# Kernel tuning notes

Measured on AMD Instinct MI355X. Metric: run time of the kernel, lower is better.

Reference implementation:

```python
import jax, jax.numpy as jnp
import numpy as np

WS = 8      # window_size
SS = 4      # shift_size
DIM = 64
B, H, W = 4, 256, 256
EPS = 1e-12


def _conv(x, w, groups=1, pad=0):
    return jax.lax.conv_general_dilated(
        x, w, window_strides=(1, 1), padding=[(pad, pad), (pad, pad)],
        feature_group_count=groups,
        dimension_numbers=('NCHW', 'OIHW', 'NCHW'))


def _window_partition(x, ws):
    # Faithful to torch: permute (B,C,nh,ws,nw,ws)->(B,C,nh,nw,ws,ws) then flat view(-1,C,ws,ws)
    b, c, h, w = x.shape
    pb, pr = (-h) % ws, (-w) % ws
    if pb or pr:
        x = jnp.pad(x, ((0, 0), (0, 0), (0, pb), (0, pr)))
    h2, w2 = h + pb, w + pr
    x = x.reshape(b, c, h2 // ws, ws, w2 // ws, ws).transpose(0, 1, 2, 4, 3, 5)
    return x.reshape(-1, c, ws, ws)


def _window_reverse(win, ws, h, w):
    pb, pr = (-h) % ws, (-w) % ws
    h2, w2 = h + pb, w + pr
    b = win.shape[0] * ws * ws // (h2 * w2)
    x = win.reshape(b, -1, h2 // ws, w2 // ws, ws, ws).transpose(0, 1, 2, 4, 3, 5)
    x = x.reshape(b, -1, h2, w2)
    return x[:, :, :h, :w]


def _chan_attn(q, k, v, temp):
    # channel (transposed) attention on flattened window pixels
    n, c = q.shape[0], q.shape[1]
    q = q.reshape(n, c, -1)
    k = k.reshape(n, c, -1)
    v = v.reshape(n, c, -1)
    q = q / jnp.maximum(jnp.linalg.norm(q, axis=-1, keepdims=True), EPS)
    k = k / jnp.maximum(jnp.linalg.norm(k, axis=-1, keepdims=True), EPS)
    attn = jax.nn.softmax(jnp.einsum('ncd,nkd->nck', q, k) / temp, axis=-1)
    out = jnp.einsum('nck,nkd->ncd', attn, v)
    return out.reshape(n, c, WS, WS)


def setup_inputs() -> dict:
    key = jax.random.key(0)
    ks = jax.random.split(key, 10)
    C = DIM
    p = lambda k, s: jax.random.normal(k, s, jnp.float32) * 0.05
    return {
        'x': jax.random.normal(ks[0], (B, C, H, W), jnp.float32),
        'x_f': jax.random.normal(ks[1], (B, C, H, W), jnp.float32),
        'temperature': jnp.ones((1,), jnp.float32),
        'qk_w': p(ks[2], (2 * C, C, 1, 1)),
        'qk_dw_w': p(ks[3], (2 * C, 1, 3, 3)),
        'v_w': p(ks[4], (C, C, 1, 1)),
        'v_dw_w': p(ks[5], (C, 1, 3, 3)),
        'proj_w': p(ks[6], (C, C, 3, 3)),
        'proj1_w': p(ks[7], (C, C, 3, 3)),
        'qkv1_w': p(ks[8], (3 * C, C, 1, 1)),
        'qkv1_dw_w': p(ks[9], (3 * C, 1, 3, 3)),
    }


def reference(x, x_f, temperature, qk_w, qk_dw_w, v_w, v_dw_w,
              proj_w, proj1_w, qkv1_w, qkv1_dw_w):
    b, c, h, w = x.shape
    xw = _window_partition(x, WS)
    xfw = _window_partition(x_f, WS)

    qk = _conv(_conv(xfw, qk_w), qk_dw_w, groups=2 * c, pad=1)
    v = _conv(_conv(xw, v_w), v_dw_w, groups=c, pad=1)
    q, k = jnp.split(qk, 2, axis=1)
    out = _chan_attn(q, k, v, temperature)
    out = _conv(out, proj_w, pad=1)
    out = _window_reverse(out, WS, h, w)

    shift = jnp.roll(out, (-SS, -SS), axis=(2, 3))
    sw = _window_partition(shift, WS)
    qkv = _conv(_conv(sw, qkv1_w), qkv1_dw_w, groups=3 * c, pad=1)
    q, k, v = jnp.split(qkv, 3, axis=1)
    out = _chan_attn(q, k, v, temperature)
    out = _conv(out, proj1_w, pad=1)
    out = _window_reverse(out, WS, h, w)
    out = jnp.roll(out, (SS, SS), axis=(2, 3))
    return out
```

## Files before the change

### kernel.cpp

```cpp
#include <hip/hip_runtime.h>

typedef short v8s __attribute__((ext_vector_type(8)));
typedef float v4f __attribute__((ext_vector_type(4)));
typedef unsigned short u16;

#define MFMA_B16(a, b, c) __builtin_amdgcn_mfma_f32_16x16x32_bf16((a), (b), (c), 0, 0, 0)
#define XS 72

__device__ __forceinline__ u16 bfr(float x) {
    unsigned u = __float_as_uint(x);
    u += 0x7fffu + ((u >> 16) & 1u);
    return (u16)(u >> 16);
}
__device__ __forceinline__ u16 f16r(float x) {
    _Float16 h = (_Float16)x; u16 u; __builtin_memcpy(&u, &h, 2); return u;
}
__device__ __forceinline__ float f16f(u16 u) {
    _Float16 h; __builtin_memcpy(&h, &u, 2); return (float)h;
}

__device__ __forceinline__ void mm_stage(const u16* __restrict__ Ag,
                                         const u16* __restrict__ XB,
                                         u16* __restrict__ M,
                                         int wv, int L, int q)
{
    v4f C[4];
#pragma unroll
    for (int nt = 0; nt < 4; ++nt) C[nt] = (v4f){0.f, 0.f, 0.f, 0.f};
#pragma unroll
    for (int kt = 0; kt < 2; ++kt) {
        v8s a = *(const v8s*)(Ag + (16 * wv + L) * 64 + kt * 32 + q * 8);
#pragma unroll
        for (int nt = 0; nt < 4; ++nt) {
            v8s b = *(const v8s*)(XB + (nt * 16 + L) * XS + kt * 32 + q * 8);
            C[nt] = MFMA_B16(a, b, C[nt]);
        }
    }
    const int rowb = 16 * wv + 4 * q;
#pragma unroll
    for (int r = 0; r < 4; ++r)
#pragma unroll
        for (int nt = 0; nt < 4; ++nt)
            M[(rowb + r) * XS + nt * 16 + L] = f16r(C[nt][r]);
}

__device__ __forceinline__ void dw_read(const u16* __restrict__ M, int c, int r0,
                                        v8s raw[4])
{
#pragma unroll
    for (int r = 0; r < 4; ++r) {
        const int rr = r0 - 1 + r;
        raw[r] = ((unsigned)rr < 8u) ? *(const v8s*)(M + c * XS + rr * 8)
                                     : (v8s){0, 0, 0, 0, 0, 0, 0, 0};
    }
}

template <bool TR, bool NORM>
__device__ __forceinline__ void dw_write(const float* __restrict__ dwg,
                                         const v8s raw[4], int c, int r0,
                                         u16* __restrict__ Out)
{
    float w[9];
#pragma unroll
    for (int k = 0; k < 9; ++k) w[k] = dwg[c * 9 + k];
    float in[4][10];
#pragma unroll
    for (int r = 0; r < 4; ++r) {
        in[r][0] = 0.f; in[r][9] = 0.f;
#pragma unroll
        for (int j = 0; j < 8; ++j) in[r][j + 1] = f16f((u16)raw[r][j]);
    }
    float o[2][8];
#pragma unroll
    for (int rr = 0; rr < 2; ++rr)
#pragma unroll
        for (int j = 0; j < 8; ++j) {
            float s;
            s = w[0] * in[rr][j];
            s = fmaf(w[1], in[rr][j + 1], s);
            s = fmaf(w[2], in[rr][j + 2], s);
            s = fmaf(w[3], in[rr + 1][j], s);
            s = fmaf(w[4], in[rr + 1][j + 1], s);
            s = fmaf(w[5], in[rr + 1][j + 2], s);
            s = fmaf(w[6], in[rr + 2][j], s);
            s = fmaf(w[7], in[rr + 2][j + 1], s);
            s = fmaf(w[8], in[rr + 2][j + 2], s);
            o[rr][j] = s;
        }
    if (NORM) {
        float ss = 0.f;
#pragma unroll
        for (int rr = 0; rr < 2; ++rr)
#pragma unroll
            for (int j = 0; j < 8; ++j) ss = fmaf(o[rr][j], o[rr][j], ss);
        ss += __shfl_xor(ss, 1);
        ss += __shfl_xor(ss, 2);
        const float sc = 1.0f / fmaxf(sqrtf(ss), 1e-12f);
#pragma unroll
        for (int rr = 0; rr < 2; ++rr)
#pragma unroll
            for (int j = 0; j < 8; ++j) o[rr][j] *= sc;
    }
    if (TR) {
#pragma unroll
        for (int rr = 0; rr < 2; ++rr)
#pragma unroll
            for (int j = 0; j < 8; ++j)
                Out[((r0 + rr) * 8 + j) * XS + c] = bfr(o[rr][j]);
    } else {
#pragma unroll
        for (int rr = 0; rr < 2; ++rr) {
            v8s v;
#pragma unroll
            for (int j = 0; j < 8; ++j) v[j] = (short)bfr(o[rr][j]);
            *(v8s*)(Out + c * XS + (r0 + rr) * 8) = v;
        }
    }
}

__device__ __forceinline__ void mm_lds(const u16* __restrict__ Am,
                                       const u16* __restrict__ Bm,
                                       int wv, int L, int q, v4f C[4])
{
#pragma unroll
    for (int nt = 0; nt < 4; ++nt) C[nt] = (v4f){0.f, 0.f, 0.f, 0.f};
#pragma unroll
    for (int kt = 0; kt < 2; ++kt) {
        v8s a = *(const v8s*)(Am + (16 * wv + L) * XS + kt * 32 + q * 8);
#pragma unroll
        for (int nt = 0; nt < 4; ++nt) {
            v8s b = *(const v8s*)(Bm + (nt * 16 + L) * XS + kt * 32 + q * 8);
            C[nt] = MFMA_B16(a, b, C[nt]);
        }
    }
}

__device__ __forceinline__ void proj_mm(const u16* __restrict__ Wg,
                                        const u16* __restrict__ Ot,
                                        int wv, int L, int q, v4f C[4])
{
#pragma unroll
    for (int nt = 0; nt < 4; ++nt) C[nt] = (v4f){0.f, 0.f, 0.f, 0.f};
    const u16* arow = Wg + (16 * wv + L) * 576;
    const int pc = L & 7;
    const int prb = L >> 3;
#pragma unroll
    for (int tap = 0; tap < 9; ++tap) {
        const int dy = tap / 3 - 1, dx = tap % 3 - 1;
        const int spc = pc + dx;
        const bool vc = (unsigned)spc < 8u;
#pragma unroll
        for (int half = 0; half < 2; ++half) {
            v8s a = *(const v8s*)(arow + tap * 64 + half * 32 + q * 8);
#pragma unroll
            for (int nt = 0; nt < 4; ++nt) {
                const int spr = nt * 2 + prb + dy;
                v8s b = {0, 0, 0, 0, 0, 0, 0, 0};
                if (vc && (unsigned)spr < 8u)
                    b = *(const v8s*)(Ot + (spr * 8 + spc) * XS + half * 32 + q * 8);
                C[nt] = MFMA_B16(a, b, C[nt]);
            }
        }
    }
}

__device__ __forceinline__ void softmax_to_lds(v4f S[4], float invt,
                                               u16* __restrict__ Am,
                                               int rowb, int L)
{
#pragma unroll
    for (int nt = 0; nt < 4; ++nt) S[nt] *= invt;
#pragma unroll
    for (int r = 0; r < 4; ++r) {
        float mx = fmaxf(fmaxf(S[0][r], S[1][r]), fmaxf(S[2][r], S[3][r]));
        mx = fmaxf(mx, __shfl_xor(mx, 1));
        mx = fmaxf(mx, __shfl_xor(mx, 2));
        mx = fmaxf(mx, __shfl_xor(mx, 4));
        mx = fmaxf(mx, __shfl_xor(mx, 8));
        float e0 = __expf(S[0][r] - mx);
        float e1 = __expf(S[1][r] - mx);
        float e2 = __expf(S[2][r] - mx);
        float e3 = __expf(S[3][r] - mx);
        float sm = e0 + e1 + e2 + e3;
        sm += __shfl_xor(sm, 1);
        sm += __shfl_xor(sm, 2);
        sm += __shfl_xor(sm, 4);
        sm += __shfl_xor(sm, 8);
        const float ri = 1.0f / sm;
        Am[(rowb + r) * XS + L +  0] = bfr(e0 * ri);
        Am[(rowb + r) * XS + L + 16] = bfr(e1 * ri);
        Am[(rowb + r) * XS + L + 32] = bfr(e2 * ri);
        Am[(rowb + r) * XS + L + 48] = bfr(e3 * ri);
    }
}

__global__ void prep(const float* __restrict__ qk_w, const float* __restrict__ v_w,
                     const float* __restrict__ qkv_w, const float* __restrict__ pw0,
                     const float* __restrict__ pw1, u16* __restrict__ Wb)
{
    int i = blockIdx.x * 256 + threadIdx.x;
    float v;
    if (i < 8192) v = qk_w[i];
    else if (i < 12288) v = v_w[i - 8192];
    else if (i < 24576) v = qkv_w[i - 12288];
    else {
        int j = i - 24576;
        const float* s = pw0;
        if (j >= 36864) { s = pw1; j -= 36864; }
        const int o = j / 576, kk = j % 576;
        const int tap = kk >> 6, c = kk & 63;
        v = s[o * 576 + c * 9 + tap];
    }
    Wb[i] = bfr(v);
}

__global__ __launch_bounds__(256, 4) void k1(
    const float* __restrict__ x, const float* __restrict__ xf,
    const float* __restrict__ temp_p,
    const float* __restrict__ qk_dw, const float* __restrict__ v_dw,
    const u16* __restrict__ Wqk, const u16* __restrict__ Wv,
    const u16* __restrict__ Wp0,
    u16* __restrict__ midb)
{
    __shared__ u16 B0[64 * XS], B1[64 * XS], B2[64 * XS], B3[64 * XS];
    const int t = threadIdx.x, n = blockIdx.x;
    const int lane = t & 63, wv = t >> 6, L = lane & 15, q = lane >> 4;
    const int rowb = 16 * wv + 4 * q;
    const size_t base = (size_t)n << 12;
    const float invt = 1.0f / temp_p[0];
    const int yp = t >> 4, xx0 = (t & 15) << 4;
    const int c2b = (yp >> 3) << 5, ir = (yp & 7) << 3;
    const int dc = t >> 2, dr0 = (t & 3) << 1;

    float4 rx[4];
    {
        const float* sf = xf + base + yp * 256 + xx0;
        const float* sx = x  + base + yp * 256 + xx0;
#pragma unroll
        for (int k = 0; k < 4; ++k) {
            float4 a = *(const float4*)(sf + 4 * k);
            rx[k] = *(const float4*)(sx + 4 * k);
            const int xx = xx0 + 4 * k;
            const int c = c2b + (xx >> 3), pb = ir + (xx & 7);
            B0[(pb + 0) * XS + c] = bfr(a.x);
            B0[(pb + 1) * XS + c] = bfr(a.y);
            B0[(pb + 2) * XS + c] = bfr(a.z);
            B0[(pb + 3) * XS + c] = bfr(a.w);
        }
    }
    __syncthreads();
    mm_stage(Wqk,        B0, B1, wv, L, q);
    mm_stage(Wqk + 4096, B0, B2, wv, L, q);
    __syncthreads();
    {
#pragma unroll
        for (int k = 0; k < 4; ++k) {
            const int xx = xx0 + 4 * k;
            const int c = c2b + (xx >> 3), pb = ir + (xx & 7);
            B3[(pb + 0) * XS + c] = bfr(rx[k].x);
            B3[(pb + 1) * XS + c] = bfr(rx[k].y);
            B3[(pb + 2) * XS + c] = bfr(rx[k].z);
            B3[(pb + 3) * XS + c] = bfr(rx[k].w);
        }
    }
    v8s rawA[4];
    dw_read(B1, dc, dr0, rawA);
    __syncthreads();
    mm_stage(Wv, B3, B0, wv, L, q);
    dw_write<false, true>(qk_dw, rawA, dc, dr0, B1);
    v8s rawB[4];
    dw_read(B2, dc, dr0, rawB);
    __syncthreads();
    dw_write<false, true>(qk_dw + 576, rawB, dc, dr0, B2);
    dw_read(B0, dc, dr0, rawA);
    dw_write<true, false>(v_dw, rawA, dc, dr0, B3);
    __syncthreads();
    v4f S[4];
    mm_lds(B1, B2, wv, L, q, S);
    softmax_to_lds(S, invt, B1, rowb, L);
    __syncthreads();
    v4f O[4];
    mm_lds(B1, B3, wv, L, q, O);
#pragma unroll
    for (int nt = 0; nt < 4; ++nt)
#pragma unroll
        for (int r = 0; r < 4; ++r)
            B2[(L + 16 * nt) * XS + rowb + r] = bfr(O[nt][r]);
    __syncthreads();
    v4f C[4];
    proj_mm(Wp0, B2, wv, L, q, C);
#pragma unroll
    for (int nt = 0; nt < 4; ++nt)
#pragma unroll
        for (int r = 0; r < 4; ++r) {
            const int o = rowb + r, p = L + 16 * nt;
            const int yy = ((o >> 5) << 3) + (p >> 3);
            const int xp = ((o & 31) << 3) + (p & 7);
            midb[base + yy * 256 + xp] = bfr(C[nt][r]);
        }
}

__global__ __launch_bounds__(256, 4) void k2(
    const u16* __restrict__ midb, const float* __restrict__ temp_p,
    const float* __restrict__ qkv_dw,
    const u16* __restrict__ Wqkv, const u16* __restrict__ Wp1,
    float* __restrict__ out)
{
    __shared__ u16 B0[64 * XS], B1[64 * XS], B2[64 * XS], B3[64 * XS];
    const int t = threadIdx.x, m = blockIdx.x;
    const int lane = t & 63, wv = t >> 6, L = lane & 15, q = lane >> 4;
    const int rowb = 16 * wv + 4 * q;
    const int plane = m >> 4, mh2 = m & 15;
    const u16* img = midb + ((size_t)plane << 16);
    const float invt = 1.0f / temp_p[0];
    const int yp = t >> 4, xx0 = (t & 15) << 4;
    const int c2b = (yp >> 3) << 5, ir = (yp & 7) << 3;
    const int dc = t >> 2, dr0 = (t & 3) << 1;

    {
        const int row = (mh2 * 16 + 4 + yp) & 255;
#pragma unroll
        for (int k = 0; k < 4; ++k) {
            const int cc = (xx0 + 4 + 4 * k) & 255;
            ushort4 a = *(const ushort4*)(img + row * 256 + cc);
            const int xx = xx0 + 4 * k;
            const int c = c2b + (xx >> 3), pb = ir + (xx & 7);
            B0[(pb + 0) * XS + c] = a.x;
            B0[(pb + 1) * XS + c] = a.y;
            B0[(pb + 2) * XS + c] = a.z;
            B0[(pb + 3) * XS + c] = a.w;
        }
    }
    __syncthreads();
    mm_stage(Wqkv,        B0, B1, wv, L, q);
    mm_stage(Wqkv + 4096, B0, B2, wv, L, q);
    mm_stage(Wqkv + 8192, B0, B3, wv, L, q);
    __syncthreads();
    v8s rawV[4];
    dw_read(B3, dc, dr0, rawV);
    dw_write<true, false>(qkv_dw + 1152, rawV, dc, dr0, B0);
    v8s rawQ[4];
    dw_read(B1, dc, dr0, rawQ);
    __syncthreads();
    dw_write<false, true>(qkv_dw, rawQ, dc, dr0, B1);
    v8s rawK[4];
    dw_read(B2, dc, dr0, rawK);
    __syncthreads();
    dw_write<false, true>(qkv_dw + 576, rawK, dc, dr0, B2);
    __syncthreads();
    v4f S[4];
    mm_lds(B1, B2, wv, L, q, S);
    softmax_to_lds(S, invt, B1, rowb, L);
    __syncthreads();
    v4f O[4];
    mm_lds(B1, B0, wv, L, q, O);
#pragma unroll
    for (int nt = 0; nt < 4; ++nt)
#pragma unroll
        for (int r = 0; r < 4; ++r)
            B3[(L + 16 * nt) * XS + rowb + r] = bfr(O[nt][r]);
    __syncthreads();
    v4f C[4];
    proj_mm(Wp1, B3, wv, L, q, C);
    float* op = out + ((size_t)plane << 16);
#pragma unroll
    for (int nt = 0; nt < 4; ++nt)
#pragma unroll
        for (int r = 0; r < 4; ++r) {
            const int o = rowb + r, p = L + 16 * nt;
            const int R = mh2 * 16 + ((o >> 5) << 3) + (p >> 3);
            const int orow = (R + 4) & 255;
            const int ocol = ((o & 31) * 8 + (p & 7) + 4) & 255;
            op[orow * 256 + ocol] = C[nt][r];
        }
}

extern "C" void kernel_launch(void* const* d_in, const int* in_sizes, int n_in,
                              void* d_out, int out_size, void* d_ws, size_t ws_size,
                              hipStream_t stream)
{
    const float* x       = (const float*)d_in[0];
    const float* xf      = (const float*)d_in[1];
    const float* temp    = (const float*)d_in[2];
    const float* qk_w    = (const float*)d_in[3];
    const float* qk_dw   = (const float*)d_in[4];
    const float* v_w     = (const float*)d_in[5];
    const float* v_dw    = (const float*)d_in[6];
    const float* proj_w  = (const float*)d_in[7];
    const float* proj1_w = (const float*)d_in[8];
    const float* qkv1_w  = (const float*)d_in[9];
    const float* qkv1_dw = (const float*)d_in[10];
    float* out = (float*)d_out;

    u16* midb = (u16*)d_ws;
    u16* Wb   = (u16*)((char*)d_ws + 33554432);

    prep<<<384, 256, 0, stream>>>(qk_w, v_w, qkv1_w, proj_w, proj1_w, Wb);
    k1<<<4096, 256, 0, stream>>>(x, xf, temp, qk_dw, v_dw,
                                 Wb, Wb + 8192, Wb + 24576, midb);
    k2<<<4096, 256, 0, stream>>>(midb, temp, qkv1_dw,
                                 Wb + 12288, Wb + 61440, out);
}
```

Baseline: 293.4 us.

## Replace padded LDS tiles with XOR-swizzled unpadded layout and raise occupancy

Removes the 72-element row padding from all shared-memory tiles and uses an XOR swizzle on 8-element chunks to avoid bank conflicts. This shrinks LDS per block from 36KB to 32KB. Launch bounds go from 4 to 5 blocks per CU so more blocks can be resident. The swizzle adds index arithmetic on every LDS access, and the tighter register budget could cause spills.

```diff
diff --git a/kernel.cpp b/kernel.cpp
--- a/kernel.cpp
+++ b/kernel.cpp
@@ -5,7 +5,14 @@
 typedef unsigned short u16;
 
 #define MFMA_B16(a, b, c) __builtin_amdgcn_mfma_f32_16x16x32_bf16((a), (b), (c), 0, 0, 0)
-#define XS 72
+
+__device__ __forceinline__ int swz8(int r) { return (r ^ (r >> 3)) & 7; }
+__device__ __forceinline__ int idxv(int r, int c8) {
+    return (r << 6) + ((c8 ^ swz8(r)) << 3);
+}
+__device__ __forceinline__ int idxs(int r, int c) {
+    return (r << 6) + ((((c >> 3) ^ swz8(r)) << 3) | (c & 7));
+}
 
 __device__ __forceinline__ u16 bfr(float x) {
     unsigned u = __float_as_uint(x);
@@ -32,7 +39,7 @@
         v8s a = *(const v8s*)(Ag + (16 * wv + L) * 64 + kt * 32 + q * 8);
 #pragma unroll
         for (int nt = 0; nt < 4; ++nt) {
-            v8s b = *(const v8s*)(XB + (nt * 16 + L) * XS + kt * 32 + q * 8);
+            v8s b = *(const v8s*)(XB + idxv(nt * 16 + L, kt * 4 + q));
             C[nt] = MFMA_B16(a, b, C[nt]);
         }
     }
@@ -41,7 +48,7 @@
     for (int r = 0; r < 4; ++r)
 #pragma unroll
         for (int nt = 0; nt < 4; ++nt)
-            M[(rowb + r) * XS + nt * 16 + L] = f16r(C[nt][r]);
+            M[idxs(rowb + r, nt * 16 + L)] = f16r(C[nt][r]);
 }
 
 __device__ __forceinline__ void dw_read(const u16* __restrict__ M, int c, int r0,
@@ -50,7 +57,7 @@
 #pragma unroll
     for (int r = 0; r < 4; ++r) {
         const int rr = r0 - 1 + r;
-        raw[r] = ((unsigned)rr < 8u) ? *(const v8s*)(M + c * XS + rr * 8)
+        raw[r] = ((unsigned)rr < 8u) ? *(const v8s*)(M + idxv(c, rr))
                                      : (v8s){0, 0, 0, 0, 0, 0, 0, 0};
     }
 }
@@ -106,14 +113,14 @@
         for (int rr = 0; rr < 2; ++rr)
 #pragma unroll
             for (int j = 0; j < 8; ++j)
-                Out[((r0 + rr) * 8 + j) * XS + c] = bfr(o[rr][j]);
+                Out[idxs((r0 + rr) * 8 + j, c)] = bfr(o[rr][j]);
     } else {
 #pragma unroll
         for (int rr = 0; rr < 2; ++rr) {
             v8s v;
 #pragma unroll
             for (int j = 0; j < 8; ++j) v[j] = (short)bfr(o[rr][j]);
-            *(v8s*)(Out + c * XS + (r0 + rr) * 8) = v;
+            *(v8s*)(Out + idxv(c, r0 + rr)) = v;
         }
     }
 }
@@ -126,10 +133,10 @@
     for (int nt = 0; nt < 4; ++nt) C[nt] = (v4f){0.f, 0.f, 0.f, 0.f};
 #pragma unroll
     for (int kt = 0; kt < 2; ++kt) {
-        v8s a = *(const v8s*)(Am + (16 * wv + L) * XS + kt * 32 + q * 8);
+        v8s a = *(const v8s*)(Am + idxv(16 * wv + L, kt * 4 + q));
 #pragma unroll
         for (int nt = 0; nt < 4; ++nt) {
-            v8s b = *(const v8s*)(Bm + (nt * 16 + L) * XS + kt * 32 + q * 8);
+            v8s b = *(const v8s*)(Bm + idxv(nt * 16 + L, kt * 4 + q));
             C[nt] = MFMA_B16(a, b, C[nt]);
         }
     }
@@ -157,7 +164,7 @@
                 const int spr = nt * 2 + prb + dy;
                 v8s b = {0, 0, 0, 0, 0, 0, 0, 0};
                 if (vc && (unsigned)spr < 8u)
-                    b = *(const v8s*)(Ot + (spr * 8 + spc) * XS + half * 32 + q * 8);
+                    b = *(const v8s*)(Ot + idxv(spr * 8 + spc, half * 4 + q));
                 C[nt] = MFMA_B16(a, b, C[nt]);
             }
         }
@@ -187,10 +194,10 @@
         sm += __shfl_xor(sm, 4);
         sm += __shfl_xor(sm, 8);
         const float ri = 1.0f / sm;
-        Am[(rowb + r) * XS + L +  0] = bfr(e0 * ri);
-        Am[(rowb + r) * XS + L + 16] = bfr(e1 * ri);
-        Am[(rowb + r) * XS + L + 32] = bfr(e2 * ri);
-        Am[(rowb + r) * XS + L + 48] = bfr(e3 * ri);
+        Am[idxs(rowb + r, L +  0)] = bfr(e0 * ri);
+        Am[idxs(rowb + r, L + 16)] = bfr(e1 * ri);
+        Am[idxs(rowb + r, L + 32)] = bfr(e2 * ri);
+        Am[idxs(rowb + r, L + 48)] = bfr(e3 * ri);
     }
 }
 
@@ -214,7 +221,7 @@
     Wb[i] = bfr(v);
 }
 
-__global__ __launch_bounds__(256, 4) void k1(
+__global__ __launch_bounds__(256, 5) void k1(
     const float* __restrict__ x, const float* __restrict__ xf,
     const float* __restrict__ temp_p,
     const float* __restrict__ qk_dw, const float* __restrict__ v_dw,
@@ -222,7 +229,7 @@
     const u16* __restrict__ Wp0,
     u16* __restrict__ midb)
 {
-    __shared__ u16 B0[64 * XS], B1[64 * XS], B2[64 * XS], B3[64 * XS];
+    __shared__ u16 B0[64 * 64], B1[64 * 64], B2[64 * 64], B3[64 * 64];
     const int t = threadIdx.x, n = blockIdx.x;
     const int lane = t & 63, wv = t >> 6, L = lane & 15, q = lane >> 4;
     const int rowb = 16 * wv + 4 * q;
@@ -242,10 +249,10 @@
             rx[k] = *(const float4*)(sx + 4 * k);
             const int xx = xx0 + 4 * k;
             const int c = c2b + (xx >> 3), pb = ir + (xx & 7);
-            B0[(pb + 0) * XS + c] = bfr(a.x);
-            B0[(pb + 1) * XS + c] = bfr(a.y);
-            B0[(pb + 2) * XS + c] = bfr(a.z);
-            B0[(pb + 3) * XS + c] = bfr(a.w);
+            B0[idxs(pb + 0, c)] = bfr(a.x);
+            B0[idxs(pb + 1, c)] = bfr(a.y);
+            B0[idxs(pb + 2, c)] = bfr(a.z);
+            B0[idxs(pb + 3, c)] = bfr(a.w);
         }
     }
     __syncthreads();
@@ -257,10 +264,10 @@
         for (int k = 0; k < 4; ++k) {
             const int xx = xx0 + 4 * k;
             const int c = c2b + (xx >> 3), pb = ir + (xx & 7);
-            B3[(pb + 0) * XS + c] = bfr(rx[k].x);
-            B3[(pb + 1) * XS + c] = bfr(rx[k].y);
-            B3[(pb + 2) * XS + c] = bfr(rx[k].z);
-            B3[(pb + 3) * XS + c] = bfr(rx[k].w);
+            B3[idxs(pb + 0, c)] = bfr(rx[k].x);
+            B3[idxs(pb + 1, c)] = bfr(rx[k].y);
+            B3[idxs(pb + 2, c)] = bfr(rx[k].z);
+            B3[idxs(pb + 3, c)] = bfr(rx[k].w);
         }
     }
     v8s rawA[4];
@@ -285,7 +292,7 @@
     for (int nt = 0; nt < 4; ++nt)
 #pragma unroll
         for (int r = 0; r < 4; ++r)
-            B2[(L + 16 * nt) * XS + rowb + r] = bfr(O[nt][r]);
+            B2[idxs(L + 16 * nt, rowb + r)] = bfr(O[nt][r]);
     __syncthreads();
     v4f C[4];
     proj_mm(Wp0, B2, wv, L, q, C);
@@ -300,13 +307,13 @@
         }
 }
 
-__global__ __launch_bounds__(256, 4) void k2(
+__global__ __launch_bounds__(256, 5) void k2(
     const u16* __restrict__ midb, const float* __restrict__ temp_p,
     const float* __restrict__ qkv_dw,
     const u16* __restrict__ Wqkv, const u16* __restrict__ Wp1,
     float* __restrict__ out)
 {
-    __shared__ u16 B0[64 * XS], B1[64 * XS], B2[64 * XS], B3[64 * XS];
+    __shared__ u16 B0[64 * 64], B1[64 * 64], B2[64 * 64], B3[64 * 64];
     const int t = threadIdx.x, m = blockIdx.x;
     const int lane = t & 63, wv = t >> 6, L = lane & 15, q = lane >> 4;
     const int rowb = 16 * wv + 4 * q;
@@ -325,10 +332,10 @@
             ushort4 a = *(const ushort4*)(img + row * 256 + cc);
             const int xx = xx0 + 4 * k;
             const int c = c2b + (xx >> 3), pb = ir + (xx & 7);
-            B0[(pb + 0) * XS + c] = a.x;
-            B0[(pb + 1) * XS + c] = a.y;
-            B0[(pb + 2) * XS + c] = a.z;
-            B0[(pb + 3) * XS + c] = a.w;
+            B0[idxs(pb + 0, c)] = a.x;
+            B0[idxs(pb + 1, c)] = a.y;
+            B0[idxs(pb + 2, c)] = a.z;
+            B0[idxs(pb + 3, c)] = a.w;
         }
     }
     __syncthreads();
@@ -358,7 +365,7 @@
     for (int nt = 0; nt < 4; ++nt)
 #pragma unroll
         for (int r = 0; r < 4; ++r)
-            B3[(L + 16 * nt) * XS + rowb + r] = bfr(O[nt][r]);
+            B3[idxs(L + 16 * nt, rowb + r)] = bfr(O[nt][r]);
     __syncthreads();
     v4f C[4];
     proj_mm(Wp1, B3, wv, L, q, C);
```

Result: slower. 351.3 us (+19.7%).
